# Performance work log

Hardware: AMD Instinct MI355X
Metric: run time of the kernel (lower is better)

The kernel has to match this reference:

```python
import jax, jax.numpy as jnp
import numpy as np

NUM_HEADS = 16

def setup_inputs() -> dict:
    key = jax.random.key(0)
    ks = jax.random.split(key, 3)
    B, S, D = 2, 2048, 1024
    x = jax.random.normal(ks[0], (B, S, D), dtype=jnp.float32)
    # xavier-uniform style scaling for weights
    Wqkv = jax.random.normal(ks[1], (3 * D, D), dtype=jnp.float32) * (1.0 / jnp.sqrt(D))
    bqkv = jnp.zeros((3 * D,), dtype=jnp.float32)
    Wo = jax.random.normal(ks[2], (D, D), dtype=jnp.float32) * (1.0 / jnp.sqrt(D))
    bo = jnp.zeros((D,), dtype=jnp.float32)
    return {"x": x, "Wqkv": Wqkv, "bqkv": bqkv, "Wo": Wo, "bo": bo}

def reference(x, Wqkv, bqkv, Wo, bo):
    B, S, D = x.shape
    H = NUM_HEADS
    hd = D // H
    # qkv projection (torch Linear: x @ W.T + b)
    qkv = x @ Wqkv.T + bqkv                      # [B, S, 3D]
    qkv = qkv.reshape(B, S, H, 3 * hd).transpose(0, 2, 1, 3)  # [B, H, S, 3hd]
    q, k, v = jnp.split(qkv, 3, axis=-1)         # each [B, H, S, hd]
    scale = 1.0 / jnp.sqrt(jnp.asarray(hd, dtype=x.dtype))
    logits = jnp.einsum('bhqd,bhkd->bhqk', q, k) * scale  # [B, H, S, S]
    attn = jax.nn.softmax(logits, axis=-1)
    vals = jnp.einsum('bhqk,bhkd->bhqd', attn, v)         # [B, H, S, hd]
    vals = vals.transpose(0, 2, 1, 3).reshape(B, S, D)
    return vals @ Wo.T + bo
```

## Files before the change

kernel.cpp:

```cpp
#include <hip/hip_runtime.h>


typedef short short8 __attribute__((ext_vector_type(8)));
typedef unsigned short ushort8v __attribute__((ext_vector_type(8)));
typedef unsigned short ushort4v __attribute__((ext_vector_type(4)));
typedef float floatx4 __attribute__((ext_vector_type(4)));

#define S_LEN 2048
#define D_MODEL 1024
#define N_HEADS 16
#define HEAD_DIM 64

#define EXP2F(x) __builtin_amdgcn_exp2f(x)

__device__ inline float bf2f(unsigned int u16) {
    union { unsigned int i; float f; } v; v.i = u16 << 16; return v.f;
}
__device__ inline unsigned short f2b(float f) {
    union { float f; unsigned int u; } v; v.f = f;
    return (unsigned short)((v.u + 0x7FFFu + ((v.u >> 16) & 1u)) >> 16);
}
__device__ inline unsigned int fbits(float f) {
    union { float f; unsigned int u; } v; v.f = f; return v.u;
}
__device__ inline unsigned int pack_bf2(float lo, float hi) {
    return __byte_perm(fbits(lo) + 0x8000u, fbits(hi) + 0x8000u, 0x7632);
}

__device__ inline int key128(int c) {
    return (c & 0x63) | ((c & 0x0C) << 1) | ((c & 0x10) >> 2);
}

__device__ inline void gld_lds16(const unsigned short* g, unsigned short* lds) {
    __builtin_amdgcn_global_load_lds(
        (const __attribute__((address_space(1))) void*)g,
        (__attribute__((address_space(3))) void*)lds, 16, 0, 0);
}

__global__ __launch_bounds__(256)
void cvt3(const float* __restrict__ s0, const float* __restrict__ s1,
          const float* __restrict__ s2,
          unsigned short* __restrict__ d0, unsigned short* __restrict__ d1,
          unsigned short* __restrict__ d2,
          int n0, int n1, int n2) {
    const int total = n0 + n1 + n2;
    for (int g = blockIdx.x * blockDim.x + threadIdx.x; g < total;
         g += gridDim.x * blockDim.x) {
        const float* s; unsigned short* d; int l;
        if (g < n0)            { s = s0; d = d0; l = g; }
        else if (g < n0 + n1)  { s = s1; d = d1; l = g - n0; }
        else                   { s = s2; d = d2; l = g - n0 - n1; }
        const float4* sp = (const float4*)s + (size_t)l * 2;
        float4 f0 = sp[0], f1 = sp[1];
        ushort8v o;
        o[0] = f2b(f0.x); o[1] = f2b(f0.y); o[2] = f2b(f0.z); o[3] = f2b(f0.w);
        o[4] = f2b(f1.x); o[5] = f2b(f1.y); o[6] = f2b(f1.z); o[7] = f2b(f1.w);
        *(ushort8v*)(d + (size_t)l * 8) = o;
    }
}

__device__ inline void gemm_core(const unsigned short* __restrict__ A,
                                 const unsigned short* __restrict__ W,
                                 int m0, int n0, int K,
                                 unsigned short* As, unsigned short* Bs,
                                 floatx4 acc[4][4]) {
    const int tid  = threadIdx.x;
    const int lane = tid & 63;
    const int wave = tid >> 6;
    const int wm = wave >> 1, wn = wave & 1;
    const int r = lane & 15, q = lane >> 4;

    const int grow = wave * 32 + (lane >> 3);
    const int gcol = (lane & 7) * 8;

    for (int k0 = 0; k0 < K; k0 += 64) {
        __syncthreads();
#pragma unroll
        for (int j = 0; j < 4; j++) {
            gld_lds16(A + (size_t)(m0 + grow + j * 8) * K + k0 + gcol,
                      As + wave * 2048 + j * 512);
            gld_lds16(W + (size_t)(n0 + grow + j * 8) * K + k0 + gcol,
                      Bs + wave * 2048 + j * 512);
        }
        __builtin_amdgcn_s_waitcnt(0);
        __syncthreads();
#pragma unroll
        for (int kk = 0; kk < 64; kk += 32) {
            short8 aF[4], bF[4];
#pragma unroll
            for (int t = 0; t < 4; t++)
                aF[t] = *(const short8*)(As + (wm * 64 + t * 16 + r) * 64 + kk + q * 8);
#pragma unroll
            for (int t = 0; t < 4; t++)
                bF[t] = *(const short8*)(Bs + (wn * 64 + t * 16 + r) * 64 + kk + q * 8);
#pragma unroll
            for (int i = 0; i < 4; i++)
#pragma unroll
                for (int j = 0; j < 4; j++)
                    acc[i][j] = __builtin_amdgcn_mfma_f32_16x16x32_bf16(aF[i], bF[j], acc[i][j], 0, 0, 0);
        }
    }
}

__device__ inline void stage_u(const unsigned short* __restrict__ g, int ldk,
                               unsigned short* lds, int wave, int lane) {
    const int lr  = lane >> 3;
    const int csw = ((lane & 7) ^ lr) * 8;
    gld_lds16(g + (size_t)(wave * 8 + lr) * ldk + csw, lds + wave * 512);
}

#define STAGE_A(kk0, buf) do {                                                 \
    _Pragma("unroll")                                                          \
    for (int u = 0; u < 4; ++u)                                                \
        stage_u(Abase + (size_t)(u * 64) * K + (kk0), K,                       \
                &AS[buf][u * 4096], wave, lane);                               \
} while (0)
#define STAGE_B2(kk0, buf) do {                                 \
    stage_u(Bbase + (kk0),                    K, &BS[buf][0],    wave, lane);  \
    stage_u(Bbase + (size_t)64 * K + (kk0),   K, &BS[buf][4096], wave, lane);  \
} while (0)
#define STAGE_B1(kk0, buf) do {                                    \
    stage_u(Bbase + (size_t)128 * K + (kk0),  K, &BS[buf][8192], wave, lane);  \
} while (0)

#define QLDB(pBx) do {                                                         \
    _Pragma("unroll")                                                          \
    for (int nj = 0; nj < 3; ++nj) {                                           \
        bF[nj][0] = *(const short8*)((pBx) + nj * 1024 + co0);                 \
        bF[nj][1] = *(const short8*)((pBx) + nj * 1024 + co1);                 \
    }                                                                          \
} while (0)

#define QPHASE(pAx, mq, ...) do {                                              \
    short8 aF[2][2];                                                           \
    _Pragma("unroll")                                                          \
    for (int m2 = 0; m2 < 2; ++m2) {                                           \
        aF[m2][0] = *(const short8*)((pAx) + ((mq) * 2 + m2) * 1024 + co0);    \
        aF[m2][1] = *(const short8*)((pAx) + ((mq) * 2 + m2) * 1024 + co1);    \
    }                                                                          \
    __VA_ARGS__;                                                               \
    __builtin_amdgcn_s_barrier();                                              \
    __builtin_amdgcn_s_setprio(1);                                             \
    _Pragma("unroll")                                                          \
    for (int kk = 0; kk < 2; ++kk)                                             \
        _Pragma("unroll")                                                      \
        for (int m2 = 0; m2 < 2; ++m2)                                         \
            _Pragma("unroll")                                                  \
            for (int nj = 0; nj < 3; ++nj)                                     \
                acc[(mq) * 2 + m2][nj] = __builtin_amdgcn_mfma_f32_16x16x32_bf16( \
                    aF[m2][kk], bF[nj][kk], acc[(mq) * 2 + m2][nj], 0, 0, 0);  \
    __builtin_amdgcn_s_setprio(0);                                             \
    __builtin_amdgcn_s_barrier();                                              \
} while (0)

#define WAIT_VM3() asm volatile("s_waitcnt vmcnt(3)" ::: "memory")
#define WAIT_VM0() asm volatile("s_waitcnt vmcnt(0)" ::: "memory")

__global__ __launch_bounds__(512, 2)
void qkv_gemm(const unsigned short* __restrict__ x,
              const unsigned short* __restrict__ Wqkv,
              const float* __restrict__ bqkv,
              unsigned short* __restrict__ Qb,
              unsigned short* __restrict__ Kb,
              unsigned short* __restrict__ Vb) {
    __shared__ unsigned short AS[2][16384];
    __shared__ unsigned short BS[2][12288];

    const int tid  = threadIdx.x;
    const int lane = tid & 63;
    const int wave = tid >> 6;
    const int wm = wave >> 2;
    const int wn = wave & 3;
    const int r  = lane & 15, q2 = lane >> 4;
    const int K  = D_MODEL;

    const int idx = blockIdx.x;
    const int swz = (idx & 7) * 32 + (idx >> 3);
    const int mb = swz & 15, nb = swz >> 4;
    const int m0 = mb * 256, n0 = nb * 192;

    const unsigned short* Abase = x    + (size_t)m0 * K;
    const unsigned short* Bbase = Wqkv + (size_t)n0 * K;

    const int co0 = ((q2 ^ (r & 7)) * 8);
    const int co1 = (((q2 + 4) ^ (r & 7)) * 8);
    const unsigned short* pA0 = &AS[0][(wm * 128 + r) * 64];
    const unsigned short* pA1 = &AS[1][(wm * 128 + r) * 64];
    const unsigned short* pB0 = &BS[0][(wn * 48 + r) * 64];
    const unsigned short* pB1 = &BS[1][(wn * 48 + r) * 64];

    floatx4 acc[8][3] = {};
    short8 bF[3][2];

    STAGE_A(0, 0);
    STAGE_B2(0, 0); STAGE_B1(0, 0);
    STAGE_B2(64, 1); STAGE_B1(64, 1);
    WAIT_VM3();
    __builtin_amdgcn_s_barrier();

    for (int i = 0; i < 8; ++i) {
        const bool more = (i < 7);
        const int kA1 = i * 128 + 64;
        const int kT2 = i * 128 + 128;
        const int kT3 = i * 128 + 192;

        QLDB(pB0);
        QPHASE(pA0, 0, { STAGE_A(kA1, 1); });
        QPHASE(pA0, 1, { if (more) STAGE_B2(kT2, 0); });
        QPHASE(pA0, 2, { if (more) STAGE_B1(kT2, 0); });
        QPHASE(pA0, 3, {
            if (more) { WAIT_VM3(); } else { WAIT_VM0(); }
        });
        QLDB(pB1);
        QPHASE(pA1, 0, { if (more) STAGE_A(kT2, 0); });
        QPHASE(pA1, 1, { if (more) STAGE_B2(kT3, 1); });
        QPHASE(pA1, 2, { if (more) STAGE_B1(kT3, 1); });
        QPHASE(pA1, 3, {
            if (more) { WAIT_VM3(); }
        });
    }

#pragma unroll
    for (int mi = 0; mi < 8; mi++) {
#pragma unroll
        for (int nj = 0; nj < 3; nj++) {
            int rem = wn * 48 + nj * 16 + r;
            int n = n0 + rem;
            int typ = rem >> 6;
            int d = rem & 63;
            float bv = bqkv[n];
            int m = m0 + wm * 128 + mi * 16 + q2 * 4;
            int b = m >> 11, s = m & 2047;
            if (typ == 2) {
                ushort4v pk;
#pragma unroll
                for (int rg = 0; rg < 4; rg++) pk[rg] = f2b(acc[mi][nj][rg] + bv);
                *(ushort4v*)(Vb + ((size_t)((b * N_HEADS + nb) * HEAD_DIM + d)) * S_LEN + s) = pk;
            } else {
                unsigned short* dst = (typ == 0) ? Qb : Kb;
                float sc = (typ == 0) ? 0.180336880f : 1.0f;
#pragma unroll
                for (int rg = 0; rg < 4; rg++)
                    dst[(((size_t)(b * N_HEADS + nb)) * S_LEN + s + rg) * HEAD_DIM + d] =
                        f2b((acc[mi][nj][rg] + bv) * sc);
            }
        }
    }
}

__global__ __launch_bounds__(256)
void out_gemm(const unsigned short* __restrict__ vals,
              const unsigned short* __restrict__ Wo,
              const float* __restrict__ bo,
              float* __restrict__ out) {
    __shared__ unsigned short As[128 * 64];
    __shared__ unsigned short Bs[128 * 64];
    const int lane = threadIdx.x & 63;
    const int wave = threadIdx.x >> 6;
    const int wm = wave >> 1, wn = wave & 1;
    const int r = lane & 15, q = lane >> 4;
    const int m0 = blockIdx.y * 128;
    const int n0 = blockIdx.x * 128;

    floatx4 acc[4][4] = {};
    gemm_core(vals, Wo, m0, n0, D_MODEL, As, Bs, acc);

#pragma unroll
    for (int i = 0; i < 4; i++) {
#pragma unroll
        for (int j = 0; j < 4; j++) {
            int n = n0 + wn * 64 + j * 16 + r;
            float bv = bo[n];
#pragma unroll
            for (int rg = 0; rg < 4; rg++) {
                int m = m0 + wm * 64 + i * 16 + q * 4 + rg;
                out[(size_t)m * D_MODEL + n] = acc[i][j][rg] + bv;
            }
        }
    }
}

__global__ __launch_bounds__(256, 2)
void attn_kernel(const unsigned short* __restrict__ Qb,
                 const unsigned short* __restrict__ Kb,
                 const unsigned short* __restrict__ Vg,
                 unsigned short* __restrict__ vals) {
    __shared__ unsigned short Ks[2 * 128 * 64];
    __shared__ unsigned short Vts[2 * 128 * 64];

    const int tid = threadIdx.x;
    const int lane = tid & 63;
    const int wave = tid >> 6;
    const int r = lane & 15, q2 = lane >> 4;
    const int r7 = r & 7;
    const int w32 = wave * 32;

    const int idx  = blockIdx.x;
    const int xcd  = idx & 7;
    const int slot = idx >> 3;
    const int bh   = (xcd << 2) | (slot >> 4);
    const int q0   = (slot & 15) * 128;
    const int b = bh >> 4, h = bh & 15;

    const unsigned short* Qp = Qb + (size_t)bh * S_LEN * HEAD_DIM;
    const unsigned short* Kp = Kb + (size_t)bh * S_LEN * HEAD_DIM;
    const unsigned short* Vp = Vg + (size_t)bh * HEAD_DIM * S_LEN;

    const int srow = lane >> 3;
    const int scol = ((lane & 7) ^ srow) * 8;

    int krow[4], vd[4], vpan[4];
#pragma unroll
    for (int t = 0; t < 4; t++) {
        int c = wave * 32 + t * 8 + srow;
        krow[t] = key128(c);
        vpan[t] = c >> 6;
        vd[t]   = c & 63;
    }

    {
        const int qrow = tid >> 1;
        const int c0 = (tid & 1) * 4;
#pragma unroll
        for (int cc = 0; cc < 4; cc++) {
            int cb = c0 + cc;
            const uint4* gq = (const uint4*)(Qp + (size_t)(q0 + qrow) * HEAD_DIM + cb * 8);
            *(uint4*)(Ks + qrow * 64 + ((cb ^ (qrow & 7)) * 8)) = *gq;
        }
    }
    __syncthreads();
    short8 qf[2][2];
#pragma unroll
    for (int nt = 0; nt < 2; nt++)
#pragma unroll
        for (int ks = 0; ks < 2; ks++) {
            int cb = ks * 4 + q2;
            qf[nt][ks] = *(const short8*)(Ks + (w32 + nt * 16 + r) * 64 + ((cb ^ r7) * 8));
        }
    __syncthreads();

#pragma unroll
    for (int t = 0; t < 4; t++) {
        gld_lds16(Kp + (size_t)krow[t] * HEAD_DIM + scol,
                  Ks + (wave * 32 + t * 8) * 64);
        gld_lds16(Vp + (size_t)vd[t] * S_LEN + vpan[t] * 64 + scol,
                  Vts + (wave * 32 + t * 8) * 64);
    }
    __builtin_amdgcn_s_waitcnt(0);
    __syncthreads();

    union { unsigned int u[4]; short8 s; } onesu;
    onesu.u[0] = 0x3F803F80u; onesu.u[1] = 0x3F803F80u;
    onesu.u[2] = 0x3F803F80u; onesu.u[3] = 0x3F803F80u;
    const short8 onesf = onesu.s;

    floatx4 l_acc[2] = {};
    floatx4 o_acc[2][4] = {};
    int cur = 0;

    for (int kt = 0; kt < S_LEN; kt += 128) {
        const int more = (kt + 128 < S_LEN);
        if (more) {
            const int nxt = (cur ^ 1) * 8192;
#pragma unroll
            for (int t = 0; t < 4; t++) {
                gld_lds16(Kp + (size_t)(kt + 128 + krow[t]) * HEAD_DIM + scol,
                          Ks + nxt + (wave * 32 + t * 8) * 64);
                gld_lds16(Vp + (size_t)vd[t] * S_LEN + kt + 128 + vpan[t] * 64 + scol,
                          Vts + nxt + (wave * 32 + t * 8) * 64);
            }
        }
        const int co = cur * 8192;

        floatx4 sp[8][2] = {};
        __builtin_amdgcn_s_setprio(1);
#pragma unroll
        for (int mt = 0; mt < 8; mt++)
#pragma unroll
            for (int ks = 0; ks < 2; ks++) {
                int cb = ks * 4 + q2;
                short8 kfr = *(const short8*)(Ks + co + (mt * 16 + r) * 64 + ((cb ^ r7) * 8));
#pragma unroll
                for (int nt = 0; nt < 2; nt++)
                    sp[mt][nt] = __builtin_amdgcn_mfma_f32_16x16x32_bf16(kfr, qf[nt][ks], sp[mt][nt], 0, 0, 0);
            }
        __builtin_amdgcn_s_setprio(0);

#pragma unroll
        for (int nt = 0; nt < 2; nt++)
#pragma unroll
            for (int mt = 0; mt < 8; mt++)
#pragma unroll
                for (int reg = 0; reg < 4; reg++)
                    sp[mt][nt][reg] = EXP2F(sp[mt][nt][reg]);

        short8 pa[2][4];
#pragma unroll
        for (int nt = 0; nt < 2; nt++)
#pragma unroll
            for (int ks = 0; ks < 4; ks++) {
                union { unsigned int u[4]; short8 s; } tw;
                tw.u[0] = pack_bf2(sp[2 * ks][nt][0],     sp[2 * ks][nt][1]);
                tw.u[1] = pack_bf2(sp[2 * ks][nt][2],     sp[2 * ks][nt][3]);
                tw.u[2] = pack_bf2(sp[2 * ks + 1][nt][0], sp[2 * ks + 1][nt][1]);
                tw.u[3] = pack_bf2(sp[2 * ks + 1][nt][2], sp[2 * ks + 1][nt][3]);
                pa[nt][ks] = tw.s;
            }

        __builtin_amdgcn_s_setprio(1);
#pragma unroll
        for (int dt = 0; dt < 4; dt++) {
            short8 vf[4];
#pragma unroll
            for (int ks = 0; ks < 4; ks++) {
                int cb = (ks & 1) * 4 + q2;
                vf[ks] = *(const short8*)(Vts + co + (ks >> 1) * 4096 + (dt * 16 + r) * 64 + ((cb ^ r7) * 8));
            }
#pragma unroll
            for (int nt = 0; nt < 2; nt++)
#pragma unroll
                for (int ks = 0; ks < 4; ks++)
                    o_acc[nt][dt] = __builtin_amdgcn_mfma_f32_16x16x32_bf16(pa[nt][ks], vf[ks], o_acc[nt][dt], 0, 0, 0);
        }
#pragma unroll
        for (int nt = 0; nt < 2; nt++)
#pragma unroll
            for (int ks = 0; ks < 4; ks++)
                l_acc[nt] = __builtin_amdgcn_mfma_f32_16x16x32_bf16(pa[nt][ks], onesf, l_acc[nt], 0, 0, 0);
        __builtin_amdgcn_s_setprio(0);

        if (more) {
            __builtin_amdgcn_s_waitcnt(0);
            __syncthreads();
            cur ^= 1;
        }
    }

#pragma unroll
    for (int nt = 0; nt < 2; nt++) {
#pragma unroll
        for (int reg = 0; reg < 4; reg++) {
            float inv = 1.0f / l_acc[nt][reg];
            int srow2 = q0 + w32 + nt * 16 + q2 * 4 + reg;
            size_t base = ((size_t)b * S_LEN + srow2) * D_MODEL + h * HEAD_DIM + r;
#pragma unroll
            for (int dt = 0; dt < 4; dt++)
                vals[base + dt * 16] = f2b(o_acc[nt][dt][reg] * inv);
        }
    }
}

extern "C" void kernel_launch(void* const* d_in, const int* in_sizes, int n_in,
                              void* d_out, int out_size, void* d_ws, size_t ws_size,
                              hipStream_t stream) {
    const float* x    = (const float*)d_in[0];
    const float* Wqkv = (const float*)d_in[1];
    const float* bqkv = (const float*)d_in[2];
    const float* Wo   = (const float*)d_in[3];
    const float* bo   = (const float*)d_in[4];
    float* out = (float*)d_out;

    const size_t NX = 4194304, NW = 3145728, NO = 1048576;
    unsigned short* xb    = (unsigned short*)d_ws;
    unsigned short* Wqkvb = xb + NX;
    unsigned short* Wob   = Wqkvb + NW;
    unsigned short* Qb    = Wob + NO;
    unsigned short* Kb    = Qb + NX;
    unsigned short* Vb    = Kb + NX;
    unsigned short* vals  = xb;

    cvt3<<<4096, 256, 0, stream>>>(x, Wqkv, Wo, xb, Wqkvb, Wob,
                                   (int)(NX / 8), (int)(NW / 8), (int)(NO / 8));
    qkv_gemm<<<256, 512, 0, stream>>>(xb, Wqkvb, bqkv, Qb, Kb, Vb);
    attn_kernel<<<512, 256, 0, stream>>>(Qb, Kb, Vb, vals);
    out_gemm<<<dim3(8, 32), 256, 0, stream>>>(vals, Wob, bo, out);
}
```

Baseline: 180.3 us.

## Load V fragments directly from global into registers instead of via LDS

Removes the double-buffered V tile in shared memory and has each wave read its V MFMA operands straight from global memory into registers at the start of each key block. This halves LDS usage and drops the LDS write and read traffic for V, which may allow more occupancy. In exchange, each of the four waves redundantly reads the same V tile from global/L2. The register footprint also grows, and the load latency is exposed inside the loop rather than hidden by the async prefetch.

```diff
diff --git a/kernel.cpp b/kernel.cpp
--- a/kernel.cpp
+++ b/kernel.cpp
@@ -286,7 +286,6 @@
                  const unsigned short* __restrict__ Vg,
                  unsigned short* __restrict__ vals) {
     __shared__ unsigned short Ks[2 * 128 * 64];
-    __shared__ unsigned short Vts[2 * 128 * 64];
 
     const int tid = threadIdx.x;
     const int lane = tid & 63;
@@ -308,15 +307,10 @@
 
     const int srow = lane >> 3;
     const int scol = ((lane & 7) ^ srow) * 8;
-
-    int krow[4], vd[4], vpan[4];
-#pragma unroll
-    for (int t = 0; t < 4; t++) {
-        int c = wave * 32 + t * 8 + srow;
-        krow[t] = key128(c);
-        vpan[t] = c >> 6;
-        vd[t]   = c & 63;
-    }
+    int krow[4];
+#pragma unroll
+    for (int t = 0; t < 4; t++)
+        krow[t] = key128(wave * 32 + t * 8 + srow);
 
     {
         const int qrow = tid >> 1;
@@ -340,12 +334,9 @@
     __syncthreads();
 
 #pragma unroll
-    for (int t = 0; t < 4; t++) {
+    for (int t = 0; t < 4; t++)
         gld_lds16(Kp + (size_t)krow[t] * HEAD_DIM + scol,
                   Ks + (wave * 32 + t * 8) * 64);
-        gld_lds16(Vp + (size_t)vd[t] * S_LEN + vpan[t] * 64 + scol,
-                  Vts + (wave * 32 + t * 8) * 64);
-    }
     __builtin_amdgcn_s_waitcnt(0);
     __syncthreads();
 
@@ -360,15 +351,22 @@
 
     for (int kt = 0; kt < S_LEN; kt += 128) {
         const int more = (kt + 128 < S_LEN);
+
+        short8 vfr[4][4];
+#pragma unroll
+        for (int dt = 0; dt < 4; dt++)
+#pragma unroll
+            for (int ks = 0; ks < 4; ks++)
+                vfr[dt][ks] = *(const short8*)(
+                    Vp + (size_t)(dt * 16 + r) * S_LEN + kt
+                       + (ks >> 1) * 64 + ((ks & 1) * 4 + q2) * 8);
+
         if (more) {
             const int nxt = (cur ^ 1) * 8192;
 #pragma unroll
-            for (int t = 0; t < 4; t++) {
+            for (int t = 0; t < 4; t++)
                 gld_lds16(Kp + (size_t)(kt + 128 + krow[t]) * HEAD_DIM + scol,
                           Ks + nxt + (wave * 32 + t * 8) * 64);
-                gld_lds16(Vp + (size_t)vd[t] * S_LEN + kt + 128 + vpan[t] * 64 + scol,
-                          Vts + nxt + (wave * 32 + t * 8) * 64);
-            }
         }
         const int co = cur * 8192;
 
@@ -409,19 +407,12 @@
 
         __builtin_amdgcn_s_setprio(1);
 #pragma unroll
-        for (int dt = 0; dt < 4; dt++) {
-            short8 vf[4];
-#pragma unroll
-            for (int ks = 0; ks < 4; ks++) {
-                int cb = (ks & 1) * 4 + q2;
-                vf[ks] = *(const short8*)(Vts + co + (ks >> 1) * 4096 + (dt * 16 + r) * 64 + ((cb ^ r7) * 8));
-            }
+        for (int dt = 0; dt < 4; dt++)
 #pragma unroll
             for (int nt = 0; nt < 2; nt++)
 #pragma unroll
                 for (int ks = 0; ks < 4; ks++)
-                    o_acc[nt][dt] = __builtin_amdgcn_mfma_f32_16x16x32_bf16(pa[nt][ks], vf[ks], o_acc[nt][dt], 0, 0, 0);
-        }
+                    o_acc[nt][dt] = __builtin_amdgcn_mfma_f32_16x16x32_bf16(pa[nt][ks], vfr[dt][ks], o_acc[nt][dt], 0, 0, 0);
 #pragma unroll
         for (int nt = 0; nt < 2; nt++)
 #pragma unroll
```

Result: slower. 209.6 us (+16.3%).

## Double-buffer and XOR-swizzle LDS tiles in output projection GEMM

Applied to the files above, without the earlier changes.

Replaces the shared gemm_core in the output projection with an inlined loop that double-buffers the A and B tiles in LDS. The next K-tile is prefetched while MFMAs run on the current one, and the per-iteration pre-load barrier is removed. Columns are XOR-swizzled by row to reduce LDS bank conflicts on the fragment reads. LDS use doubles to 64KB per block, which may lower occupancy.

```diff
diff --git a/kernel.cpp b/kernel.cpp
--- a/kernel.cpp
+++ b/kernel.cpp
@@ -56,49 +56,6 @@
         o[0] = f2b(f0.x); o[1] = f2b(f0.y); o[2] = f2b(f0.z); o[3] = f2b(f0.w);
         o[4] = f2b(f1.x); o[5] = f2b(f1.y); o[6] = f2b(f1.z); o[7] = f2b(f1.w);
         *(ushort8v*)(d + (size_t)l * 8) = o;
-    }
-}
-
-__device__ inline void gemm_core(const unsigned short* __restrict__ A,
-                                 const unsigned short* __restrict__ W,
-                                 int m0, int n0, int K,
-                                 unsigned short* As, unsigned short* Bs,
-                                 floatx4 acc[4][4]) {
-    const int tid  = threadIdx.x;
-    const int lane = tid & 63;
-    const int wave = tid >> 6;
-    const int wm = wave >> 1, wn = wave & 1;
-    const int r = lane & 15, q = lane >> 4;
-
-    const int grow = wave * 32 + (lane >> 3);
-    const int gcol = (lane & 7) * 8;
-
-    for (int k0 = 0; k0 < K; k0 += 64) {
-        __syncthreads();
-#pragma unroll
-        for (int j = 0; j < 4; j++) {
-            gld_lds16(A + (size_t)(m0 + grow + j * 8) * K + k0 + gcol,
-                      As + wave * 2048 + j * 512);
-            gld_lds16(W + (size_t)(n0 + grow + j * 8) * K + k0 + gcol,
-                      Bs + wave * 2048 + j * 512);
-        }
-        __builtin_amdgcn_s_waitcnt(0);
-        __syncthreads();
-#pragma unroll
-        for (int kk = 0; kk < 64; kk += 32) {
-            short8 aF[4], bF[4];
-#pragma unroll
-            for (int t = 0; t < 4; t++)
-                aF[t] = *(const short8*)(As + (wm * 64 + t * 16 + r) * 64 + kk + q * 8);
-#pragma unroll
-            for (int t = 0; t < 4; t++)
-                bF[t] = *(const short8*)(Bs + (wn * 64 + t * 16 + r) * 64 + kk + q * 8);
-#pragma unroll
-            for (int i = 0; i < 4; i++)
-#pragma unroll
-                for (int j = 0; j < 4; j++)
-                    acc[i][j] = __builtin_amdgcn_mfma_f32_16x16x32_bf16(aF[i], bF[j], acc[i][j], 0, 0, 0);
-        }
     }
 }
 
@@ -253,17 +210,71 @@
               const unsigned short* __restrict__ Wo,
               const float* __restrict__ bo,
               float* __restrict__ out) {
-    __shared__ unsigned short As[128 * 64];
-    __shared__ unsigned short Bs[128 * 64];
-    const int lane = threadIdx.x & 63;
-    const int wave = threadIdx.x >> 6;
+    __shared__ unsigned short As[2][8192];
+    __shared__ unsigned short Bs[2][8192];
+
+    const int tid  = threadIdx.x;
+    const int lane = tid & 63;
+    const int wave = tid >> 6;
     const int wm = wave >> 1, wn = wave & 1;
-    const int r = lane & 15, q = lane >> 4;
+    const int r = lane & 15, q2 = lane >> 4;
+    const int K = D_MODEL;
     const int m0 = blockIdx.y * 128;
     const int n0 = blockIdx.x * 128;
 
+    const unsigned short* Abase = vals + (size_t)m0 * K;
+    const unsigned short* Bbase = Wo   + (size_t)n0 * K;
+
+    const int lr  = lane >> 3;
+    const int csw = ((lane & 7) ^ lr) * 8;
+
+    const int co0 = ((q2 ^ (r & 7)) * 8);
+    const int co1 = (((q2 + 4) ^ (r & 7)) * 8);
+
     floatx4 acc[4][4] = {};
-    gemm_core(vals, Wo, m0, n0, D_MODEL, As, Bs, acc);
+
+#define OSTAGE(gbase, k0, lds) do {                                            \
+    _Pragma("unroll")                                                          \
+    for (int u = 0; u < 4; ++u)                                                \
+        gld_lds16((gbase) + (size_t)(u * 32 + wave * 8 + lr) * K + (k0) + csw, \
+                  (lds) + u * 2048 + wave * 512);                              \
+} while (0)
+
+    OSTAGE(Abase, 0, &As[0][0]);
+    OSTAGE(Bbase, 0, &Bs[0][0]);
+    __builtin_amdgcn_s_waitcnt(0);
+    __syncthreads();
+
+    int buf = 0;
+    for (int k0 = 0; k0 < K; k0 += 64) {
+        const bool more = (k0 + 64 < K);
+        if (more) {
+            OSTAGE(Abase, k0 + 64, &As[buf ^ 1][0]);
+            OSTAGE(Bbase, k0 + 64, &Bs[buf ^ 1][0]);
+        }
+#pragma unroll
+        for (int kk = 0; kk < 2; kk++) {
+            const int co = kk ? co1 : co0;
+            short8 aF[4], bF[4];
+#pragma unroll
+            for (int t = 0; t < 4; t++)
+                aF[t] = *(const short8*)(&As[buf][(wm * 64 + t * 16 + r) * 64] + co);
+#pragma unroll
+            for (int t = 0; t < 4; t++)
+                bF[t] = *(const short8*)(&Bs[buf][(wn * 64 + t * 16 + r) * 64] + co);
+#pragma unroll
+            for (int i = 0; i < 4; i++)
+#pragma unroll
+                for (int j = 0; j < 4; j++)
+                    acc[i][j] = __builtin_amdgcn_mfma_f32_16x16x32_bf16(aF[i], bF[j], acc[i][j], 0, 0, 0);
+        }
+        if (more) {
+            __builtin_amdgcn_s_waitcnt(0);
+            __syncthreads();
+            buf ^= 1;
+        }
+    }
+#undef OSTAGE
 
 #pragma unroll
     for (int i = 0; i < 4; i++) {
@@ -273,7 +284,7 @@
             float bv = bo[n];
 #pragma unroll
             for (int rg = 0; rg < 4; rg++) {
-                int m = m0 + wm * 64 + i * 16 + q * 4 + rg;
+                int m = m0 + wm * 64 + i * 16 + q2 * 4 + rg;
                 out[(size_t)m * D_MODEL + n] = acc[i][j][rg] + bv;
             }
         }
```

New measurement: 176.5 us. 2.1% less time.
